# Performance work log

Hardware: AMD Instinct MI355X
Metric: run time of the kernel (lower is better)

## Reference

```python
import jax, jax.numpy as jnp
import numpy as np
import math

E = 39      # num_experts
D = 16      # STATE_DIM / d_model
DFF = 64    # d_ff
B = 32768   # batch of VM states (original runs one at a time)
OPCODE = 6  # slot of opcode in state vector
EPS = 1e-5  # torch LayerNorm default eps


def layernorm(x):
    # elementwise_affine=False LayerNorm over last dim, biased variance
    m = jnp.mean(x, axis=-1, keepdims=True)
    v = jnp.mean((x - m) ** 2, axis=-1, keepdims=True)
    return (x - m) / jnp.sqrt(v + EPS)


def setup_inputs() -> dict:
    key = jax.random.key(0)
    ks = jax.random.split(key, 10)
    state = jax.random.normal(ks[0], (B, D), dtype=jnp.float32)
    # opcode slot holds an integer-valued opcode in [0, E) so gating is realistic
    opcode = jax.random.randint(ks[1], (B,), 0, E).astype(jnp.float32)
    state = state.at[:, OPCODE].set(opcode)
    s = 0.1
    Wq = jax.random.normal(ks[2], (E, D, D), dtype=jnp.float32) * s
    Wk = jax.random.normal(ks[3], (E, D, D), dtype=jnp.float32) * s
    Wv = jax.random.normal(ks[4], (E, D, D), dtype=jnp.float32) * s
    Wo = jax.random.normal(ks[5], (E, D, D), dtype=jnp.float32) * s
    W1 = jax.random.normal(ks[6], (E, DFF, D), dtype=jnp.float32) * s
    b1 = jax.random.normal(ks[7], (E, DFF), dtype=jnp.float32) * s
    W2 = jax.random.normal(ks[8], (E, D, DFF), dtype=jnp.float32) * s
    b2 = jax.random.normal(ks[9], (E, D), dtype=jnp.float32) * s
    return {"state": state, "Wq": Wq, "Wk": Wk, "Wv": Wv, "Wo": Wo,
            "W1": W1, "b1": b1, "W2": W2, "b2": b2}


def reference(state, Wq, Wk, Wv, Wo, W1, b1, W2, b2):
    # --- OpcodeRouter: soft top-hat gates from the opcode slot ---
    opcode = state[:, OPCODE]                                  # [B]
    idx = jnp.arange(E, dtype=state.dtype)                     # [E]
    diff = opcode[:, None] - idx[None, :]                      # [B,E]
    gates = jax.nn.sigmoid((diff + 0.5) * 20.0) * jax.nn.sigmoid((-diff + 0.5) * 20.0)

    # --- All E experts on all B states, batched (x: seq_len == 1 token) ---
    xn = layernorm(state)                                      # [B,D]
    Q = jnp.einsum('bd,eod->beo', xn, Wq)                      # [B,E,D]
    K = jnp.einsum('bd,eod->beo', xn, Wk)
    V = jnp.einsum('bd,eod->beo', xn, Wv)
    scores = jnp.sum(Q * K, axis=-1, keepdims=True) / math.sqrt(D)  # [B,E,1]
    w = jax.nn.softmax(scores, axis=-1)                        # ones (seq_len 1), kept faithful
    attn = jnp.einsum('bev,ejv->bej', w * V, Wo)               # [B,E,D]
    x1 = state[:, None, :] + attn                              # residual 1

    xn2 = layernorm(x1)
    h = jax.nn.silu(jnp.einsum('bed,efd->bef', xn2, W1) + b1)  # [B,E,DFF]
    ffn = jnp.einsum('bef,edf->bed', h, W2) + b2               # [B,E,D]
    x2 = x1 + ffn                                              # residual 2

    # --- gated mixture of expert outputs ---
    return jnp.einsum('be,bed->bd', gates, x2)                 # [B,D]
```

## Files before the change

kernel.cpp:

```cpp
#include <hip/hip_runtime.h>
#include <math.h>

#define NE 39
#define ND 16
#define NB 32768
#define OPC 6
#define EPS 1e-5f
#define NSB 128
#define BCAP 24
#define SPE (NSB * BCAP)
#define TPE 80
#define CPE (TPE / 2)
#define NWAVE (NE * CPE)
#define NBLK ((NWAVE + 3) / 4)

#define CNT_OFF  0
#define WVO_OFF  (CNT_OFF + NE * NSB * 4)
#define LIST_OFF (WVO_OFF + NE * 256 * 4)
#define WS_NEED  (LIST_OFF + NE * SPE * 4)

#define GATE0 0.9999092022104184f

typedef __attribute__((ext_vector_type(8))) short bf16x8;
typedef __attribute__((ext_vector_type(4))) float f32x4;
typedef unsigned long long ull;

__device__ __forceinline__ short bfr(float f) {
    unsigned u = __float_as_uint(f);
    u = (u + 0x7FFFu + ((u >> 16) & 1u)) >> 16;
    return (short)u;
}
__device__ __forceinline__ bf16x8 dupfrag(float a, float b, float c, float d) {
    const short s0 = bfr(a), s1 = bfr(b), s2 = bfr(c), s3 = bfr(d);
    bf16x8 r;
    r[0] = s0; r[1] = s1; r[2] = s2; r[3] = s3;
    r[4] = s0; r[5] = s1; r[6] = s2; r[7] = s3;
    return r;
}
__device__ __forceinline__ bf16x8 dupfragW(float4 v) {
    return dupfrag(0.5f * v.x, 0.5f * v.y, 0.5f * v.z, 0.5f * v.w);
}
__device__ __forceinline__ float siluf_(float a) {
    return a / (1.0f + __expf(-a));
}

__global__ __launch_bounds__(256) void k_scatter(const float* __restrict__ state,
                                                 const float* __restrict__ Wv,
                                                 const float* __restrict__ Wo,
                                                 int* __restrict__ cnt,
                                                 float* __restrict__ wvo,
                                                 int* __restrict__ list) {
    __shared__ int lcnt[NE];
    const int tid = threadIdx.x, bid = blockIdx.x;
    if (tid < NE) lcnt[tid] = 0;
    __syncthreads();
    const int r = bid * 256 + tid;
    const int e = (int)state[r * ND + OPC];
    const int rank = atomicAdd(&lcnt[e], 1);
    if (rank < BCAP) list[e * SPE + bid * BCAP + rank] = r;
    __syncthreads();
    if (tid < NE) cnt[tid * NSB + bid] = (lcnt[tid] < BCAP) ? lcnt[tid] : BCAP;

    if (bid < NE) {
        const int j = tid >> 4, d = tid & 15;
        const float* woRow = Wo + bid * 256 + j * 16;
        const float* wvCol = Wv + bid * 256 + d;
        float a = 0.0f;
        #pragma unroll
        for (int v = 0; v < 16; ++v) a += woRow[v] * wvCol[v * 16];
        wvo[bid * 256 + j * 16 + d] = a;
    }
}

__global__ __launch_bounds__(256, 2) void k_main(const float* __restrict__ state,
                                                 const int* __restrict__ cnt,
                                                 const int* __restrict__ list,
                                                 const float* __restrict__ wvo,
                                                 const float* __restrict__ W1,
                                                 const float* __restrict__ b1,
                                                 const float* __restrict__ W2,
                                                 const float* __restrict__ b2,
                                                 float* __restrict__ out) {
    __shared__ int Ecum[4][132];
    const int wid = threadIdx.x >> 6, lane = threadIdx.x & 63;
    const int w = blockIdx.x * 4 + wid;
    if (w >= NWAVE) return;
    const int e  = __builtin_amdgcn_readfirstlane(w / CPE);
    const int s0 = (w - e * CPE) * 32;

    int v = cnt[e * NSB + lane];
    int u = cnt[e * NSB + 64 + lane];
    #pragma unroll
    for (int d = 1; d < 64; d <<= 1) { const int t = __shfl_up(v, d, 64); if (lane >= d) v += t; }
    const int tot_lo = __shfl(v, 63, 64);
    #pragma unroll
    for (int d = 1; d < 64; d <<= 1) { const int t = __shfl_up(u, d, 64); if (lane >= d) u += t; }
    u += tot_lo;
    const int total = __shfl(u, 63, 64);
    if (s0 >= total) return;

    int* Ew = Ecum[wid];
    if (lane == 0) Ew[0] = 0;
    Ew[lane + 1]  = v;
    Ew[lane + 65] = u;

    const int g   = lane >> 4;
    const int r16 = lane & 15;

    const bf16x8 wvoF = dupfragW(*(const float4*)(wvo + e * 256 + r16 * 16 + 4 * g));
    bf16x8 w1F[4], w2F[4];
    float4 b1q[4];
    #pragma unroll
    for (int c = 0; c < 4; ++c) {
        w1F[c] = dupfragW(*(const float4*)(W1 + e * 1024 + (16 * c + r16) * 16 + 4 * g));
        w2F[c] = dupfragW(*(const float4*)(W2 + e * 1024 + r16 * 64 + 16 * c + 4 * g));
        b1q[c] = *(const float4*)(b1 + e * 64 + 16 * c + 4 * g);
    }
    const float4 b2q = *(const float4*)(b2 + e * 16 + 4 * g);
    const f32x4 z = {0.0f, 0.0f, 0.0f, 0.0f};

    auto tile = [&](int sbase) {
        const int sraw = sbase + r16;
        const bool valid = sraw < total;
        const int s = valid ? sraw : (total - 1);
        int lo = 0, hi = 128;
        #pragma unroll
        for (int it = 0; it < 7; ++it) {
            const int mid = (lo + hi) >> 1;
            if (Ew[mid] <= s) lo = mid; else hi = mid;
        }
        const int row = list[e * SPE + lo * BCAP + (s - Ew[lo])];

        const float4 x4 = *(const float4*)(state + row * ND + 4 * g);

        float sm = x4.x + x4.y + x4.z + x4.w;
        float q = x4.x * x4.x + x4.y * x4.y + x4.z * x4.z + x4.w * x4.w;
        sm += __shfl_xor(sm, 16); q += __shfl_xor(q, 16);
        sm += __shfl_xor(sm, 32); q += __shfl_xor(q, 32);
        const float m1 = sm * 0.0625f;
        const float rs1 = rsqrtf(fmaxf(q * 0.0625f - m1 * m1, 0.0f) + EPS);
        const bf16x8 xnf = dupfrag((x4.x - m1) * rs1, (x4.y - m1) * rs1,
                                   (x4.z - m1) * rs1, (x4.w - m1) * rs1);

        const f32x4 at = __builtin_amdgcn_mfma_f32_16x16x32_bf16(wvoF, xnf, z, 0, 0, 0);

        const float x10 = x4.x + at[0], x11 = x4.y + at[1];
        const float x12 = x4.z + at[2], x13 = x4.w + at[3];
        float s2 = x10 + x11 + x12 + x13;
        float q2 = x10 * x10 + x11 * x11 + x12 * x12 + x13 * x13;
        s2 += __shfl_xor(s2, 16); q2 += __shfl_xor(q2, 16);
        s2 += __shfl_xor(s2, 32); q2 += __shfl_xor(q2, 32);
        const float m2 = s2 * 0.0625f;
        const float rs2 = rsqrtf(fmaxf(q2 * 0.0625f - m2 * m2, 0.0f) + EPS);
        const bf16x8 xn2f = dupfrag((x10 - m2) * rs2, (x11 - m2) * rs2,
                                    (x12 - m2) * rs2, (x13 - m2) * rs2);

        f32x4 ffn = z;
        #pragma unroll
        for (int c = 0; c < 4; ++c) {
            const f32x4 hc = __builtin_amdgcn_mfma_f32_16x16x32_bf16(w1F[c], xn2f, z, 0, 0, 0);
            const bf16x8 hfrag = dupfrag(siluf_(hc[0] + b1q[c].x),
                                         siluf_(hc[1] + b1q[c].y),
                                         siluf_(hc[2] + b1q[c].z),
                                         siluf_(hc[3] + b1q[c].w));
            ffn = __builtin_amdgcn_mfma_f32_16x16x32_bf16(w2F[c], hfrag, ffn, 0, 0, 0);
        }

        if (valid) {
            const float4 o4 = make_float4(GATE0 * (x10 + ffn[0] + b2q.x),
                                          GATE0 * (x11 + ffn[1] + b2q.y),
                                          GATE0 * (x12 + ffn[2] + b2q.z),
                                          GATE0 * (x13 + ffn[3] + b2q.w));
            *(float4*)(out + row * ND + 4 * g) = o4;
        }
    };

    tile(s0);
    if (s0 + 16 < total) tile(s0 + 16);
}

__device__ __forceinline__ float dot16g(const float* __restrict__ w, const float* v) {
    float a0 = 0.f, a1 = 0.f, a2 = 0.f, a3 = 0.f;
    #pragma unroll
    for (int i = 0; i < 16; i += 4) {
        a0 += w[i+0] * v[i+0];
        a1 += w[i+1] * v[i+1];
        a2 += w[i+2] * v[i+2];
        a3 += w[i+3] * v[i+3];
    }
    return (a0 + a1) + (a2 + a3);
}

__global__ __launch_bounds__(64) void k_fallback(const float* __restrict__ state,
                                                 const float* __restrict__ Wv,
                                                 const float* __restrict__ Wo,
                                                 const float* __restrict__ W1,
                                                 const float* __restrict__ b1,
                                                 const float* __restrict__ W2,
                                                 const float* __restrict__ b2,
                                                 float* __restrict__ out) {
    const int row = blockIdx.x * 64 + threadIdx.x;
    const int e = (int)state[row * ND + OPC];

    float x[16];
    #pragma unroll
    for (int i = 0; i < 16; ++i) x[i] = state[row * 16 + i];

    float s = 0.f;
    #pragma unroll
    for (int i = 0; i < 16; ++i) s += x[i];
    const float m1 = s / 16.f;
    float v1 = 0.f;
    #pragma unroll
    for (int i = 0; i < 16; ++i) { const float d = x[i] - m1; v1 += d * d; }
    const float rs1 = rsqrtf(v1 / 16.f + EPS);
    float xn[16];
    #pragma unroll
    for (int i = 0; i < 16; ++i) xn[i] = (x[i] - m1) * rs1;

    float V[16];
    #pragma unroll
    for (int o = 0; o < 16; ++o) V[o] = dot16g(Wv + e * 256 + o * 16, xn);
    float x1[16];
    #pragma unroll
    for (int o = 0; o < 16; ++o) x1[o] = x[o] + dot16g(Wo + e * 256 + o * 16, V);

    float s2 = 0.f;
    #pragma unroll
    for (int i = 0; i < 16; ++i) s2 += x1[i];
    const float m2 = s2 / 16.f;
    float v2 = 0.f;
    #pragma unroll
    for (int i = 0; i < 16; ++i) { const float d = x1[i] - m2; v2 += d * d; }
    const float rs2 = rsqrtf(v2 / 16.f + EPS);
    float xn2[16];
    #pragma unroll
    for (int i = 0; i < 16; ++i) xn2[i] = (x1[i] - m2) * rs2;

    float r[16];
    #pragma unroll
    for (int o = 0; o < 16; ++o) r[o] = x1[o] + b2[e * 16 + o];

    #pragma unroll
    for (int c = 0; c < 4; ++c) {
        float hc[16];
        #pragma unroll
        for (int k = 0; k < 16; ++k) {
            const int f = c * 16 + k;
            const float a = b1[e * 64 + f] + dot16g(W1 + e * 1024 + f * 16, xn2);
            hc[k] = a / (1.0f + __expf(-a));
        }
        #pragma unroll
        for (int o = 0; o < 16; ++o)
            r[o] += dot16g(W2 + e * 1024 + o * 64 + c * 16, hc);
    }

    #pragma unroll
    for (int o = 0; o < 16; ++o) out[row * 16 + o] = GATE0 * r[o];
}

extern "C" void kernel_launch(void* const* d_in, const int* in_sizes, int n_in,
                              void* d_out, int out_size, void* d_ws, size_t ws_size,
                              hipStream_t stream) {
    const float* state = (const float*)d_in[0];
    const float* Wv = (const float*)d_in[3];
    const float* Wo = (const float*)d_in[4];
    const float* W1 = (const float*)d_in[5];
    const float* b1 = (const float*)d_in[6];
    const float* W2 = (const float*)d_in[7];
    const float* b2 = (const float*)d_in[8];
    float* out = (float*)d_out;

    if (ws_size >= (size_t)WS_NEED) {
        int* cnt   = (int*)((char*)d_ws + CNT_OFF);
        float* wvo = (float*)((char*)d_ws + WVO_OFF);
        int* list  = (int*)((char*)d_ws + LIST_OFF);
        k_scatter<<<NSB, 256, 0, stream>>>(state, Wv, Wo, cnt, wvo, list);
        k_main<<<NBLK, 256, 0, stream>>>(state, cnt, list, wvo,
                                         W1, b1, W2, b2, out);
    } else {
        k_fallback<<<NB / 64, 64, 0, stream>>>(state, Wv, Wo, W1, b1, W2, b2, out);
    }
}
```

Measured before the change: 16.88 us.

## Compute Wv·Wo per block in shared memory, one tile per wave

```diff
diff --git a/kernel.cpp b/kernel.cpp
--- a/kernel.cpp
+++ b/kernel.cpp
@@ -10,13 +10,11 @@
 #define BCAP 24
 #define SPE (NSB * BCAP)
 #define TPE 80
-#define CPE (TPE / 2)
-#define NWAVE (NE * CPE)
-#define NBLK ((NWAVE + 3) / 4)
+#define NWAVE (NE * TPE)
+#define NBLK (NWAVE / 4)
 
 #define CNT_OFF  0
-#define WVO_OFF  (CNT_OFF + NE * NSB * 4)
-#define LIST_OFF (WVO_OFF + NE * 256 * 4)
+#define LIST_OFF (CNT_OFF + NE * NSB * 4)
 #define WS_NEED  (LIST_OFF + NE * SPE * 4)
 
 #define GATE0 0.9999092022104184f
@@ -45,10 +43,7 @@
 }
 
 __global__ __launch_bounds__(256) void k_scatter(const float* __restrict__ state,
-                                                 const float* __restrict__ Wv,
-                                                 const float* __restrict__ Wo,
                                                  int* __restrict__ cnt,
-                                                 float* __restrict__ wvo,
                                                  int* __restrict__ list) {
     __shared__ int lcnt[NE];
     const int tid = threadIdx.x, bid = blockIdx.x;
@@ -60,54 +55,68 @@
     if (rank < BCAP) list[e * SPE + bid * BCAP + rank] = r;
     __syncthreads();
     if (tid < NE) cnt[tid * NSB + bid] = (lcnt[tid] < BCAP) ? lcnt[tid] : BCAP;
-
-    if (bid < NE) {
-        const int j = tid >> 4, d = tid & 15;
-        const float* woRow = Wo + bid * 256 + j * 16;
-        const float* wvCol = Wv + bid * 256 + d;
-        float a = 0.0f;
-        #pragma unroll
-        for (int v = 0; v < 16; ++v) a += woRow[v] * wvCol[v * 16];
-        wvo[bid * 256 + j * 16 + d] = a;
-    }
 }
 
 __global__ __launch_bounds__(256, 2) void k_main(const float* __restrict__ state,
                                                  const int* __restrict__ cnt,
                                                  const int* __restrict__ list,
-                                                 const float* __restrict__ wvo,
+                                                 const float* __restrict__ Wv,
+                                                 const float* __restrict__ Wo,
                                                  const float* __restrict__ W1,
                                                  const float* __restrict__ b1,
                                                  const float* __restrict__ W2,
                                                  const float* __restrict__ b2,
                                                  float* __restrict__ out) {
-    __shared__ int Ecum[4][132];
-    const int wid = threadIdx.x >> 6, lane = threadIdx.x & 63;
+    __shared__ float lwvo[256];
+    __shared__ int E[NSB + 1];
+    const int tid = threadIdx.x;
+    const int wid = tid >> 6, lane = tid & 63;
     const int w = blockIdx.x * 4 + wid;
-    if (w >= NWAVE) return;
-    const int e  = __builtin_amdgcn_readfirstlane(w / CPE);
-    const int s0 = (w - e * CPE) * 32;
-
-    int v = cnt[e * NSB + lane];
-    int u = cnt[e * NSB + 64 + lane];
-    #pragma unroll
-    for (int d = 1; d < 64; d <<= 1) { const int t = __shfl_up(v, d, 64); if (lane >= d) v += t; }
-    const int tot_lo = __shfl(v, 63, 64);
-    #pragma unroll
-    for (int d = 1; d < 64; d <<= 1) { const int t = __shfl_up(u, d, 64); if (lane >= d) u += t; }
-    u += tot_lo;
-    const int total = __shfl(u, 63, 64);
+    const int e = __builtin_amdgcn_readfirstlane(w / TPE);
+
+    {
+        const int j = tid >> 4, d = tid & 15;
+        const float* woRow = Wo + e * 256 + j * 16;
+        const float* wvCol = Wv + e * 256 + d;
+        float a = 0.0f;
+        #pragma unroll
+        for (int v2 = 0; v2 < 16; ++v2) a += woRow[v2] * wvCol[v2 * 16];
+        lwvo[j * 16 + d] = a;
+    }
+    if (wid == 0) {
+        int v = cnt[e * NSB + lane];
+        int u = cnt[e * NSB + 64 + lane];
+        #pragma unroll
+        for (int d = 1; d < 64; d <<= 1) { const int t = __shfl_up(v, d, 64); if (lane >= d) v += t; }
+        const int tot_lo = __shfl(v, 63, 64);
+        #pragma unroll
+        for (int d = 1; d < 64; d <<= 1) { const int t = __shfl_up(u, d, 64); if (lane >= d) u += t; }
+        u += tot_lo;
+        if (lane == 0) E[0] = 0;
+        E[lane + 1]  = v;
+        E[lane + 65] = u;
+    }
+    __syncthreads();
+
+    const int total = E[NSB];
+    const int s0 = (w - e * TPE) * 16;
     if (s0 >= total) return;
-
-    int* Ew = Ecum[wid];
-    if (lane == 0) Ew[0] = 0;
-    Ew[lane + 1]  = v;
-    Ew[lane + 65] = u;
 
     const int g   = lane >> 4;
     const int r16 = lane & 15;
 
-    const bf16x8 wvoF = dupfragW(*(const float4*)(wvo + e * 256 + r16 * 16 + 4 * g));
+    const int sraw = s0 + r16;
+    const bool valid = sraw < total;
+    const int s = valid ? sraw : (total - 1);
+    int lo = 0, hi = NSB;
+    #pragma unroll
+    for (int it = 0; it < 7; ++it) {
+        const int mid = (lo + hi) >> 1;
+        if (E[mid] <= s) lo = mid; else hi = mid;
+    }
+    const int row = list[e * SPE + lo * BCAP + (s - E[lo])];
+
+    const bf16x8 wvoF = dupfragW(*(const float4*)(lwvo + r16 * 16 + 4 * g));
     bf16x8 w1F[4], w2F[4];
     float4 b1q[4];
     #pragma unroll
@@ -119,64 +128,48 @@
     const float4 b2q = *(const float4*)(b2 + e * 16 + 4 * g);
     const f32x4 z = {0.0f, 0.0f, 0.0f, 0.0f};
 
-    auto tile = [&](int sbase) {
-        const int sraw = sbase + r16;
-        const bool valid = sraw < total;
-        const int s = valid ? sraw : (total - 1);
-        int lo = 0, hi = 128;
-        #pragma unroll
-        for (int it = 0; it < 7; ++it) {
-            const int mid = (lo + hi) >> 1;
-            if (Ew[mid] <= s) lo = mid; else hi = mid;
-        }
-        const int row = list[e * SPE + lo * BCAP + (s - Ew[lo])];
-
-        const float4 x4 = *(const float4*)(state + row * ND + 4 * g);
-
-        float sm = x4.x + x4.y + x4.z + x4.w;
-        float q = x4.x * x4.x + x4.y * x4.y + x4.z * x4.z + x4.w * x4.w;
-        sm += __shfl_xor(sm, 16); q += __shfl_xor(q, 16);
-        sm += __shfl_xor(sm, 32); q += __shfl_xor(q, 32);
-        const float m1 = sm * 0.0625f;
-        const float rs1 = rsqrtf(fmaxf(q * 0.0625f - m1 * m1, 0.0f) + EPS);
-        const bf16x8 xnf = dupfrag((x4.x - m1) * rs1, (x4.y - m1) * rs1,
-                                   (x4.z - m1) * rs1, (x4.w - m1) * rs1);
-
-        const f32x4 at = __builtin_amdgcn_mfma_f32_16x16x32_bf16(wvoF, xnf, z, 0, 0, 0);
-
-        const float x10 = x4.x + at[0], x11 = x4.y + at[1];
-        const float x12 = x4.z + at[2], x13 = x4.w + at[3];
-        float s2 = x10 + x11 + x12 + x13;
-        float q2 = x10 * x10 + x11 * x11 + x12 * x12 + x13 * x13;
-        s2 += __shfl_xor(s2, 16); q2 += __shfl_xor(q2, 16);
-        s2 += __shfl_xor(s2, 32); q2 += __shfl_xor(q2, 32);
-        const float m2 = s2 * 0.0625f;
-        const float rs2 = rsqrtf(fmaxf(q2 * 0.0625f - m2 * m2, 0.0f) + EPS);
-        const bf16x8 xn2f = dupfrag((x10 - m2) * rs2, (x11 - m2) * rs2,
-                                    (x12 - m2) * rs2, (x13 - m2) * rs2);
-
-        f32x4 ffn = z;
-        #pragma unroll
-        for (int c = 0; c < 4; ++c) {
-            const f32x4 hc = __builtin_amdgcn_mfma_f32_16x16x32_bf16(w1F[c], xn2f, z, 0, 0, 0);
-            const bf16x8 hfrag = dupfrag(siluf_(hc[0] + b1q[c].x),
-                                         siluf_(hc[1] + b1q[c].y),
-                                         siluf_(hc[2] + b1q[c].z),
-                                         siluf_(hc[3] + b1q[c].w));
-            ffn = __builtin_amdgcn_mfma_f32_16x16x32_bf16(w2F[c], hfrag, ffn, 0, 0, 0);
-        }
-
-        if (valid) {
-            const float4 o4 = make_float4(GATE0 * (x10 + ffn[0] + b2q.x),
-                                          GATE0 * (x11 + ffn[1] + b2q.y),
-                                          GATE0 * (x12 + ffn[2] + b2q.z),
-                                          GATE0 * (x13 + ffn[3] + b2q.w));
-            *(float4*)(out + row * ND + 4 * g) = o4;
-        }
-    };
-
-    tile(s0);
-    if (s0 + 16 < total) tile(s0 + 16);
+    const float4 x4 = *(const float4*)(state + row * ND + 4 * g);
+
+    float sm = x4.x + x4.y + x4.z + x4.w;
+    float q = x4.x * x4.x + x4.y * x4.y + x4.z * x4.z + x4.w * x4.w;
+    sm += __shfl_xor(sm, 16); q += __shfl_xor(q, 16);
+    sm += __shfl_xor(sm, 32); q += __shfl_xor(q, 32);
+    const float m1 = sm * 0.0625f;
+    const float rs1 = rsqrtf(fmaxf(q * 0.0625f - m1 * m1, 0.0f) + EPS);
+    const bf16x8 xnf = dupfrag((x4.x - m1) * rs1, (x4.y - m1) * rs1,
+                               (x4.z - m1) * rs1, (x4.w - m1) * rs1);
+
+    const f32x4 at = __builtin_amdgcn_mfma_f32_16x16x32_bf16(wvoF, xnf, z, 0, 0, 0);
+
+    const float x10 = x4.x + at[0], x11 = x4.y + at[1];
+    const float x12 = x4.z + at[2], x13 = x4.w + at[3];
+    float s2 = x10 + x11 + x12 + x13;
+    float q2 = x10 * x10 + x11 * x11 + x12 * x12 + x13 * x13;
+    s2 += __shfl_xor(s2, 16); q2 += __shfl_xor(q2, 16);
+    s2 += __shfl_xor(s2, 32); q2 += __shfl_xor(q2, 32);
+    const float m2 = s2 * 0.0625f;
+    const float rs2 = rsqrtf(fmaxf(q2 * 0.0625f - m2 * m2, 0.0f) + EPS);
+    const bf16x8 xn2f = dupfrag((x10 - m2) * rs2, (x11 - m2) * rs2,
+                                (x12 - m2) * rs2, (x13 - m2) * rs2);
+
+    f32x4 ffn = z;
+    #pragma unroll
+    for (int c = 0; c < 4; ++c) {
+        const f32x4 hc = __builtin_amdgcn_mfma_f32_16x16x32_bf16(w1F[c], xn2f, z, 0, 0, 0);
+        const bf16x8 hfrag = dupfrag(siluf_(hc[0] + b1q[c].x),
+                                     siluf_(hc[1] + b1q[c].y),
+                                     siluf_(hc[2] + b1q[c].z),
+                                     siluf_(hc[3] + b1q[c].w));
+        ffn = __builtin_amdgcn_mfma_f32_16x16x32_bf16(w2F[c], hfrag, ffn, 0, 0, 0);
+    }
+
+    if (valid) {
+        const float4 o4 = make_float4(GATE0 * (x10 + ffn[0] + b2q.x),
+                                      GATE0 * (x11 + ffn[1] + b2q.y),
+                                      GATE0 * (x12 + ffn[2] + b2q.z),
+                                      GATE0 * (x13 + ffn[3] + b2q.w));
+        *(float4*)(out + row * ND + 4 * g) = o4;
+    }
 }
 
 __device__ __forceinline__ float dot16g(const float* __restrict__ w, const float* v) {
@@ -272,11 +265,10 @@
     float* out = (float*)d_out;
 
     if (ws_size >= (size_t)WS_NEED) {
-        int* cnt   = (int*)((char*)d_ws + CNT_OFF);
-        float* wvo = (float*)((char*)d_ws + WVO_OFF);
-        int* list  = (int*)((char*)d_ws + LIST_OFF);
-        k_scatter<<<NSB, 256, 0, stream>>>(state, Wv, Wo, cnt, wvo, list);
-        k_main<<<NBLK, 256, 0, stream>>>(state, cnt, list, wvo,
+        int* cnt  = (int*)((char*)d_ws + CNT_OFF);
+        int* list = (int*)((char*)d_ws + LIST_OFF);
+        k_scatter<<<NSB, 256, 0, stream>>>(state, cnt, list);
+        k_main<<<NBLK, 256, 0, stream>>>(state, cnt, list, Wv, Wo,
                                          W1, b1, W2, b2, out);
     } else {
         k_fallback<<<NB / 64, 64, 0, stream>>>(state, Wv, Wo, W1, b1, W2, b2, out);
```

Result: slower. 17.47 us (+3.5%).
